# Performance work log

Hardware: AMD Instinct MI355X
Metric: run time of the kernel (lower is better)

The kernel has to match this reference:

```python
import jax, jax.numpy as jnp
import numpy as np

B, T, D, H = 2, 2048, 1024, 16
Dh = D // H


def _rope(q, k):
    # q, k: (B, H, T, Dh), interleaved even/odd rotation
    t = q.shape[2]
    dh = q.shape[3]
    inv_freq = 1.0 / (10000.0 ** (jnp.arange(0, dh, 2, dtype=jnp.float32) / dh))
    pos = jnp.arange(t, dtype=jnp.float32)
    freqs = pos[:, None] * inv_freq[None, :]          # (T, Dh/2)
    sin = jnp.sin(freqs)[None, None]                  # (1,1,T,Dh/2)
    cos = jnp.cos(freqs)[None, None]

    def rot(x):
        xe, xo = x[..., ::2], x[..., 1::2]
        re = xe * cos - xo * sin
        ro = xe * sin + xo * cos
        return jnp.stack([re, ro], axis=-1).reshape(x.shape)

    return rot(q), rot(k)


def setup_inputs() -> dict:
    key = jax.random.key(0)
    k1, k2, k3 = jax.random.split(key, 3)
    s = 1.0 / np.sqrt(D)
    return {
        "x": jax.random.normal(k1, (B, T, D), dtype=jnp.float32),
        "w_qkv": jax.random.normal(k2, (3 * D, D), dtype=jnp.float32) * s,
        "b_qkv": jnp.zeros((3 * D,), dtype=jnp.float32),
        "w_out": jax.random.normal(k3, (D, D), dtype=jnp.float32) * s,
        "b_out": jnp.zeros((D,), dtype=jnp.float32),
    }


def reference(x, w_qkv, b_qkv, w_out, b_out):
    b, t, d = x.shape
    qkv = x @ w_qkv.T + b_qkv                         # (B,T,3D)
    q, k, v = jnp.split(qkv, 3, axis=-1)
    q = q.reshape(b, t, H, Dh).transpose(0, 2, 1, 3)  # (B,H,T,Dh)
    k = k.reshape(b, t, H, Dh).transpose(0, 2, 1, 3)
    v = v.reshape(b, t, H, Dh).transpose(0, 2, 1, 3)
    q, k = _rope(q, k)
    scores = jnp.einsum("bhtd,bhsd->bhts", q, k) / jnp.sqrt(jnp.float32(Dh))
    causal = jnp.tril(jnp.ones((t, t), dtype=bool))[None, None]
    scores = jnp.where(causal, scores, -jnp.inf)
    probs = jax.nn.softmax(scores, axis=-1)
    out = jnp.einsum("bhts,bhsd->bhtd", probs, v)     # (B,H,T,Dh)
    out = out.transpose(0, 2, 1, 3).reshape(b, t, d)
    return out @ w_out.T + b_out
```

## Files before the change

kernel.cpp:

```cpp
#include <hip/hip_runtime.h>
#include <hip/hip_bf16.h>
#include <math.h>
#include <type_traits>

#define B_ 2
#define T_ 2048
#define D_ 1024
#define H_ 16
#define DH_ 64

typedef __bf16 bf16_t;
typedef bf16_t bf16x8 __attribute__((ext_vector_type(8)));
typedef bf16_t bf16x4 __attribute__((ext_vector_type(4)));
typedef float f32x4 __attribute__((ext_vector_type(4)));

typedef __attribute__((address_space(1))) const void gas_void;
typedef __attribute__((address_space(3))) void las_void;

__device__ __forceinline__ void gld16(const void* g, void* l) {
    __builtin_amdgcn_global_load_lds((gas_void*)g, (las_void*)l, 16, 0, 0);
}

#define WAITALL() asm volatile("s_waitcnt vmcnt(0) lgkmcnt(0)" ::: "memory")
#define BARRIER() do { asm volatile("" ::: "memory"); __builtin_amdgcn_s_barrier(); asm volatile("" ::: "memory"); } while (0)

__global__ __launch_bounds__(256) void cvt3(const float* __restrict__ a,
                                            const float* __restrict__ b,
                                            const float* __restrict__ c,
                                            bf16_t* __restrict__ oa,
                                            bf16_t* __restrict__ ob,
                                            bf16_t* __restrict__ oc,
                                            float2* __restrict__ tab) {
    if (blockIdx.x >= 8192) {
        int j = (blockIdx.x - 8192) * 256 + threadIdx.x;
        int t = j >> 5, d2 = j & 31;
        float invf = exp2f(-(float)d2 * 0.4152410118609203f);
        float ang = (float)t * invf;
        float sn, cs;
        sincosf(ang, &sn, &cs);
        tab[j] = make_float2(cs, sn);
        return;
    }
    int i = blockIdx.x * 256 + threadIdx.x;
    const float* src; bf16_t* dst; int off;
    if (i < 1048576)      { src = a; dst = oa; off = i; }
    else if (i < 1835008) { src = b; dst = ob; off = i - 1048576; }
    else                  { src = c; dst = oc; off = i - 1835008; }
    float4 f = ((const float4*)src)[off];
    bf16x4 v = { (bf16_t)f.x, (bf16_t)f.y, (bf16_t)f.z, (bf16_t)f.w };
    ((bf16x4*)dst)[off] = v;
}

__global__ __launch_bounds__(512, 4) void gemmqkv(const bf16_t* __restrict__ A,
                                                  const bf16_t* __restrict__ Bw,
                                                  const float* __restrict__ bias,
                                                  const float2* __restrict__ tab,
                                                  bf16_t* __restrict__ q_out,
                                                  bf16_t* __restrict__ k_out,
                                                  bf16_t* __restrict__ vt_out) {
    __shared__ __align__(16) char smem[65536];

    int tid = threadIdx.x;
    int lane = tid & 63, wid = tid >> 6;
    int wm = wid >> 2, wn = wid & 3;
    int lr = lane & 15, lk = lane >> 4;

    int l = blockIdx.y * 12 + blockIdx.x;
    int u = (l & 7) * 48 + (l >> 3);
    int bx = u % 12;
    int by = u / 12;

    f32x4 acc[4][4];
    f32x4 z = {0.f, 0.f, 0.f, 0.f};
#pragma unroll
    for (int i = 0; i < 4; i++)
#pragma unroll
        for (int j = 0; j < 4; j++) acc[i][j] = z;

    int cb = (tid & 3) * 16;
    int rT = tid >> 2;
    int sw = cb ^ (((rT >> 1) & 3) << 4);
    const char* gAp  = (const char*)A  + ((size_t)(by * 128 + rT)) * 2048 + sw;
    const char* gBp0 = (const char*)Bw + ((size_t)(bx * 256 + rT)) * 2048 + sw;
    const char* gBp1 = (const char*)Bw + ((size_t)(bx * 256 + 128 + rT)) * 2048 + sw;

    auto stg = [&](int par, int kt) __attribute__((always_inline)) {
        char* base = smem + par * 24576;
        gld16(gAp  + kt * 64, base + tid * 16);
        gld16(gBp0 + kt * 64, base + 8192 + tid * 16);
        gld16(gBp1 + kt * 64, base + 16384 + tid * 16);
    };

    int offA[4], offB[4];
#pragma unroll
    for (int m = 0; m < 4; m++) {
        int row = wm * 64 + m * 16 + lr;
        offA[m] = row * 64 + ((lk * 16) ^ (((row >> 1) & 3) << 4));
    }
#pragma unroll
    for (int n = 0; n < 4; n++) {
        int row = wn * 64 + n * 16 + lr;
        offB[n] = 8192 + row * 64 + ((lk * 16) ^ (((row >> 1) & 3) << 4));
    }

    stg(0, 0);
    for (int kt = 0; kt < 32; ++kt) {
        const char* buf = smem + (kt & 1) * 24576;
        WAITALL();
        BARRIER();
        if (kt < 31) stg((kt + 1) & 1, kt + 1);
        bf16x8 Af[4], Bf[4];
#pragma unroll
        for (int m = 0; m < 4; m++) Af[m] = *(const bf16x8*)(buf + offA[m]);
#pragma unroll
        for (int n = 0; n < 4; n++) Bf[n] = *(const bf16x8*)(buf + offB[n]);
        __builtin_amdgcn_s_setprio(1);
#pragma unroll
        for (int m = 0; m < 4; m++)
#pragma unroll
            for (int n = 0; n < 4; n++)
                acc[m][n] = __builtin_amdgcn_mfma_f32_16x16x32_bf16(Af[m], Bf[n], acc[m][n], 0, 0, 0);
        __builtin_amdgcn_s_setprio(0);
    }
    WAITALL();
    BARRIER();

    int m_base = by * 128 + wm * 64;
    int n_base = bx * 256 + wn * 64;
    char* myL = smem + wid * 8192;
    int which = n_base >> 10;
    int h = (n_base & 1023) >> 6;
    int b = m_base >> 11, t0 = m_base & 2047;
    int bh = b * H_ + h;
    if (which == 2) {
#pragma unroll
        for (int m = 0; m < 4; m++)
#pragma unroll
            for (int n = 0; n < 4; n++) {
                int rd = n * 16 + lr;
                float bv = bias[n_base + rd];
#pragma unroll
                for (int j = 0; j < 4; j++) {
                    int ct = m * 16 + lk * 4 + j;
                    int ct2 = (ct & 32) | (((ct >> 2) & 3) << 3) | (((ct >> 4) & 1) << 2) | (ct & 3);
                    int addr = (rd * 128 + ct2 * 2) ^ ((rd & 7) << 4);
                    *(bf16_t*)(myL + addr) = (bf16_t)(acc[m][n][j] + bv);
                }
            }
#pragma unroll
        for (int it = 0; it < 8; it++) {
            int row = it * 8 + (lane >> 3);
            int byt = (lane & 7) * 16;
            bf16x8 val = *(const bf16x8*)(myL + ((row * 128 + byt) ^ ((row & 7) << 4)));
            *(bf16x8*)(vt_out + ((size_t)bh * DH_ + row) * T_ + t0 + (lane & 7) * 8) = val;
        }
    } else {
        bf16_t* dst = which ? k_out : q_out;
        float qscl = which ? 1.0f : 0.18033688011112042f;
#pragma unroll
        for (int m = 0; m < 4; m++)
#pragma unroll
            for (int n = 0; n < 4; n++) {
                int dh = n * 16 + lr;
                float bv = bias[n_base + dh];
                int dh2 = dh >> 1;
                bool even = (dh & 1) == 0;
#pragma unroll
                for (int j = 0; j < 4; j++) {
                    int rt = m * 16 + lk * 4 + j;
                    float v = acc[m][n][j] + bv;
                    float pp = __shfl_xor(v, 1);
                    float2 cs = tab[(t0 + rt) * 32 + dh2];
                    float r = even ? v * cs.x - pp * cs.y : v * cs.x + pp * cs.y;
                    r *= qscl;
                    int addr = (rt * 128 + dh * 2) ^ ((rt & 7) << 4);
                    *(bf16_t*)(myL + addr) = (bf16_t)r;
                }
            }
#pragma unroll
        for (int it = 0; it < 8; it++) {
            int row = it * 8 + (lane >> 3);
            int byt = (lane & 7) * 16;
            bf16x8 val = *(const bf16x8*)(myL + ((row * 128 + byt) ^ ((row & 7) << 4)));
            *(bf16x8*)(dst + ((size_t)bh * T_ + t0 + row) * DH_ + (lane & 7) * 8) = val;
        }
    }
}

__global__ __launch_bounds__(256) void gemm128o(const bf16_t* __restrict__ A,
                                                const bf16_t* __restrict__ Bw,
                                                const float* __restrict__ bias,
                                                float* __restrict__ f_out,
                                                int K, int N) {
    __shared__ __align__(16) char smem[49152];
    char* b0 = smem;
    char* b1 = smem + 16384;
    char* b2 = smem + 32768;

    int tid = threadIdx.x;
    int lane = tid & 63, wid = tid >> 6;
    int wr = wid >> 1, wc = wid & 1;
    int lr = lane & 15, lk = lane >> 4;

    int l = blockIdx.y * gridDim.x + blockIdx.x;
    int chunk = (gridDim.x * gridDim.y) >> 3;
    int u = (l & 7) * chunk + (l >> 3);
    int bx = u % gridDim.x;
    int by = u / gridDim.x;

    f32x4 acc[4][4];
    f32x4 z = {0.f, 0.f, 0.f, 0.f};
#pragma unroll
    for (int i = 0; i < 4; i++)
#pragma unroll
        for (int j = 0; j < 4; j++) acc[i][j] = z;

    const char* Ab = (const char*)(A + (size_t)by * 128 * K);
    const char* Bb = (const char*)(Bw + (size_t)bx * 128 * K);
    const int rowstride = K * 2;

    int p0 = tid * 16;
    int p1 = 4096 + tid * 16;
    int r0 = p0 >> 6, r1 = p1 >> 6;
    int cb0 = (p0 & 63) ^ (((r0 >> 1) & 3) << 4);
    int cb1 = (p1 & 63) ^ (((r1 >> 1) & 3) << 4);
    size_t gA0 = (size_t)r0 * rowstride + cb0;
    size_t gA1 = (size_t)r1 * rowstride + cb1;

    int oa[4], ob[4];
#pragma unroll
    for (int m = 0; m < 4; m++) {
        int row = wr * 64 + m * 16 + lr;
        oa[m] = row * 64 + ((lk * 16) ^ (((row >> 1) & 3) << 4));
    }
#pragma unroll
    for (int n = 0; n < 4; n++) {
        int row = wc * 64 + n * 16 + lr;
        ob[n] = row * 64 + ((lk * 16) ^ (((row >> 1) & 3) << 4));
    }

    auto stg = [&](char* buf, int ks) __attribute__((always_inline)) {
        const char* Ag = Ab + (size_t)ks * 64;
        const char* Bg = Bb + (size_t)ks * 64;
        gld16(Ag + gA0, buf + p0);
        gld16(Ag + gA1, buf + p1);
        gld16(Bg + gA0, buf + 8192 + p0);
        gld16(Bg + gA1, buf + 8192 + p1);
    };

    auto iterf = [&](auto vmc, char* buf, int ks, bool dostage) __attribute__((always_inline)) {
        constexpr int VM = decltype(vmc)::value;
        if constexpr (VM == 8)      asm volatile("s_waitcnt vmcnt(8)" ::: "memory");
        else if constexpr (VM == 4) asm volatile("s_waitcnt vmcnt(4)" ::: "memory");
        else                        asm volatile("s_waitcnt vmcnt(0)" ::: "memory");
        __builtin_amdgcn_s_barrier();
        asm volatile("" ::: "memory");
        bf16x8 Af[4], Bf[4];
#pragma unroll
        for (int m = 0; m < 4; m++) Af[m] = *(const bf16x8*)(buf + oa[m]);
#pragma unroll
        for (int n = 0; n < 4; n++) Bf[n] = *(const bf16x8*)(buf + 8192 + ob[n]);
#pragma unroll
        for (int m = 0; m < 4; m++)
#pragma unroll
            for (int n = 0; n < 4; n++)
                acc[m][n] = __builtin_amdgcn_mfma_f32_16x16x32_bf16(Af[m], Bf[n], acc[m][n], 0, 0, 0);
        asm volatile("" ::: "memory");
        __builtin_amdgcn_s_barrier();
        asm volatile("" ::: "memory");
        if (dostage) stg(buf, ks);
    };

    std::integral_constant<int, 8> c8;
    std::integral_constant<int, 4> c4;
    std::integral_constant<int, 0> c0;

    stg(b0, 0);
    stg(b1, 1);
    stg(b2, 2);
    for (int s = 0; s < 30; s += 3) {
        iterf(c8, b0, s + 3, s + 3 < 32);
        iterf(c8, b1, s + 4, s + 4 < 32);
        iterf(c8, b2, s + 5, s + 5 < 32);
    }
    iterf(c4, b0, 0, false);
    iterf(c0, b1, 0, false);

    int m_base = by * 128 + wr * 64;
    int n_base = bx * 128 + wc * 64;
#pragma unroll
    for (int m = 0; m < 4; m++) {
        int gm0 = m_base + m * 16 + lk * 4;
#pragma unroll
        for (int n = 0; n < 4; n++) {
            int nc = n_base + n * 16 + lr;
            float bv = bias[nc];
#pragma unroll
            for (int j = 0; j < 4; j++)
                f_out[(size_t)(gm0 + j) * N + nc] = acc[m][n][j] + bv;
        }
    }
}

__global__ __launch_bounds__(256, 4) void attn128(const bf16_t* __restrict__ Q,
                                                  const bf16_t* __restrict__ K,
                                                  const bf16_t* __restrict__ Vt,
                                                  bf16_t* __restrict__ Ao) {
    __shared__ __align__(16) char smem[40960];

    int tid = threadIdx.x;
    int lane = tid & 63, wid = tid >> 6;
    int lr = lane & 15, lk = lane >> 4;
    int xcd = blockIdx.x & 7, idx = blockIdx.x >> 3;
    int bh = xcd * 4 + (idx & 3);
    int i4 = idx >> 2;
    int qt = (i4 < 8) ? i4 : 23 - i4;
    int q0 = qt * 128;
    int qrelw = wid * 16 + lr;

    const bf16_t* Qp0 = Q + ((size_t)bh * T_ + q0 + qrelw) * DH_;
    const bf16_t* Qp1 = Qp0 + 64 * DH_;
    bf16x8 qa0 = *(const bf16x8*)(Qp0 + lk * 8);
    bf16x8 qa1 = *(const bf16x8*)(Qp0 + 32 + lk * 8);
    bf16x8 qb0 = *(const bf16x8*)(Qp1 + lk * 8);
    bf16x8 qb1 = *(const bf16x8*)(Qp1 + 32 + lk * 8);

    f32x4 zz = {0.f, 0.f, 0.f, 0.f};
    f32x4 oa0[4], oa1[4];
#pragma unroll
    for (int dt = 0; dt < 4; dt++) { oa0[dt] = zz; oa1[dt] = zz; }
    float ls0 = 0.f, ls1 = 0.f;
    bf16x8 pA0, pA1, pB0, pB1;

    const char* Kbase = (const char*)(K + (size_t)bh * T_ * DH_);
    const char* Vbase = (const char*)(Vt + (size_t)bh * DH_ * T_);

    auto stage = [&](int s, char* Kd, char* Vd) __attribute__((always_inline)) {
        int kv0 = s * 64;
        const char* Kg = Kbase + (size_t)kv0 * 128;
#pragma unroll
        for (int c = 0; c < 2; c++) {
            int o = c * 4096 + tid * 16;
            int r = o >> 7;
            int g = o ^ ((r & 7) << 4);
            gld16(Kg + g, Kd + o);
            gld16(Vbase + (size_t)r * (T_ * 2) + kv0 * 2 + (g & 127), Vd + o);
        }
    };

    auto do_qk = [&](const char* Kc, int m0, int m1) __attribute__((always_inline)) {
#pragma unroll
        for (int kt = 0; kt < 4; kt++) {
            int row = kt * 16 + lr;
            int key = (row & 7) << 4;
            bf16x8 kf0 = *(const bf16x8*)(Kc + ((row * 128 + lk * 16) ^ key));
            bf16x8 kf1 = *(const bf16x8*)(Kc + ((row * 128 + 64 + lk * 16) ^ key));
            if (m0 != 2) {
                f32x4 s = zz;
                s = __builtin_amdgcn_mfma_f32_16x16x32_bf16(kf0, qa0, s, 0, 0, 0);
                s = __builtin_amdgcn_mfma_f32_16x16x32_bf16(kf1, qa1, s, 0, 0, 0);
#pragma unroll
                for (int j = 0; j < 4; j++) {
                    float sv = s[j];
                    if (m0 == 1) {
                        int kv = kt * 16 + lk * 4 + j;
                        sv = (kv <= qrelw) ? sv : -__builtin_inff();
                    }
                    float e = exp2f(sv);
                    ls0 += e;
                    if (kt < 2) pA0[kt * 4 + j] = (bf16_t)e;
                    else        pA1[(kt - 2) * 4 + j] = (bf16_t)e;
                }
            }
            {
                f32x4 s = zz;
                s = __builtin_amdgcn_mfma_f32_16x16x32_bf16(kf0, qb0, s, 0, 0, 0);
                s = __builtin_amdgcn_mfma_f32_16x16x32_bf16(kf1, qb1, s, 0, 0, 0);
#pragma unroll
                for (int j = 0; j < 4; j++) {
                    float sv = s[j];
                    if (m1 == 1) {
                        int kv = kt * 16 + lk * 4 + j;
                        sv = (kv <= qrelw) ? sv : -__builtin_inff();
                    }
                    float e = exp2f(sv);
                    ls1 += e;
                    if (kt < 2) pB0[kt * 4 + j] = (bf16_t)e;
                    else        pB1[(kt - 2) * 4 + j] = (bf16_t)e;
                }
            }
        }
    };

    auto do_pv = [&](const char* Vc, bool g0on) __attribute__((always_inline)) {
#pragma unroll
        for (int dt = 0; dt < 4; dt++) {
            int row = dt * 16 + lr;
            int key = (row & 7) << 4;
            bf16x8 vf0 = *(const bf16x8*)(Vc + ((row * 128 + lk * 16) ^ key));
            bf16x8 vf1 = *(const bf16x8*)(Vc + ((row * 128 + 64 + lk * 16) ^ key));
            if (g0on) {
                f32x4 o = oa0[dt];
                o = __builtin_amdgcn_mfma_f32_16x16x32_bf16(vf0, pA0, o, 0, 0, 0);
                o = __builtin_amdgcn_mfma_f32_16x16x32_bf16(vf1, pA1, o, 0, 0, 0);
                oa0[dt] = o;
            }
            f32x4 o = oa1[dt];
            o = __builtin_amdgcn_mfma_f32_16x16x32_bf16(vf0, pB0, o, 0, 0, 0);
            o = __builtin_amdgcn_mfma_f32_16x16x32_bf16(vf1, pB1, o, 0, 0, 0);
            oa1[dt] = o;
        }
    };

    stage(0, smem, smem + 16384);
    stage(1, smem + 8192, smem + 24576);
    asm volatile("s_waitcnt vmcnt(4)" ::: "memory");
    __builtin_amdgcn_s_barrier();
    asm volatile("" ::: "memory");
    do_qk(smem, qt == 0 ? 1 : 0, 0);

    char* Kr = smem + 8192;
    char* Kw = smem;
    char* Vr = smem + 16384;
    char* Vn = smem + 24576;
    char* Vw = smem + 32768;

    int last = 2 * qt;
    auto iterA = [&](int s, int m0, int m1) __attribute__((always_inline)) {
        WAITALL();
        __builtin_amdgcn_s_barrier();
        asm volatile("" ::: "memory");
        if (s + 2 <= last + 1) stage(s + 2, Kw, Vw);
        do_pv(Vr, true);
        do_qk(Kr, m0, m1);
        char* t;
        t = Kr; Kr = Kw; Kw = t;
        t = Vr; Vr = Vn; Vn = Vw; Vw = t;
    };

    for (int s = 0; s < last - 1; ++s) iterA(s, 0, 0);
    if (qt > 0) iterA(last - 1, 1, 0);
    iterA(last, 2, 1);
    do_pv(Vr, false);
    __syncthreads();

    ls0 += __shfl_xor(ls0, 16); ls0 += __shfl_xor(ls0, 32);
    ls1 += __shfl_xor(ls1, 16); ls1 += __shfl_xor(ls1, 32);
    float ri0 = __builtin_amdgcn_rcpf(ls0);
    float ri1 = __builtin_amdgcn_rcpf(ls1);

    char* myL = smem + wid * 2048;
    int b = bh >> 4, h = bh & 15;
#pragma unroll
    for (int dt = 0; dt < 4; dt++)
#pragma unroll
        for (int j = 0; j < 4; j++) {
            int dh = dt * 16 + lk * 4 + j;
            int addr = (lr * 128 + dh * 2) ^ ((lr & 7) << 4);
            *(bf16_t*)(myL + addr) = (bf16_t)(oa0[dt][j] * ri0);
        }
#pragma unroll
    for (int it = 0; it < 2; it++) {
        int row = it * 8 + (lane >> 3);
        int byt = (lane & 7) * 16;
        bf16x8 val = *(const bf16x8*)(myL + ((row * 128 + byt) ^ ((row & 7) << 4)));
        int t = q0 + wid * 16 + row;
        *(bf16x8*)(Ao + ((size_t)b * T_ + t) * D_ + h * DH_ + (lane & 7) * 8) = val;
    }
#pragma unroll
    for (int dt = 0; dt < 4; dt++)
#pragma unroll
        for (int j = 0; j < 4; j++) {
            int dh = dt * 16 + lk * 4 + j;
            int addr = (lr * 128 + dh * 2) ^ ((lr & 7) << 4);
            *(bf16_t*)(myL + addr) = (bf16_t)(oa1[dt][j] * ri1);
        }
#pragma unroll
    for (int it = 0; it < 2; it++) {
        int row = it * 8 + (lane >> 3);
        int byt = (lane & 7) * 16;
        bf16x8 val = *(const bf16x8*)(myL + ((row * 128 + byt) ^ ((row & 7) << 4)));
        int t = q0 + 64 + wid * 16 + row;
        *(bf16x8*)(Ao + ((size_t)b * T_ + t) * D_ + h * DH_ + (lane & 7) * 8) = val;
    }
}

extern "C" void kernel_launch(void* const* d_in, const int* in_sizes, int n_in,
                              void* d_out, int out_size, void* d_ws, size_t ws_size,
                              hipStream_t stream) {
    const float* x     = (const float*)d_in[0];
    const float* w_qkv = (const float*)d_in[1];
    const float* b_qkv = (const float*)d_in[2];
    const float* w_out = (const float*)d_in[3];
    const float* b_out = (const float*)d_in[4];
    float* out = (float*)d_out;

    char* ws = (char*)d_ws;
    bf16_t* xb    = (bf16_t*)(ws);
    bf16_t* wqkvb = (bf16_t*)(ws + 8388608);
    bf16_t* wob   = (bf16_t*)(ws + 14680064);
    bf16_t* qb    = (bf16_t*)(ws + 16777216);
    bf16_t* kb    = (bf16_t*)(ws + 25165824);
    bf16_t* vtb   = (bf16_t*)(ws + 33554432);
    bf16_t* ab    = (bf16_t*)(ws + 41943040);
    float2* tab   = (float2*)(ws + 41943040);

    cvt3<<<8448, 256, 0, stream>>>(x, w_qkv, w_out, xb, wqkvb, wob, tab);

    gemmqkv<<<dim3(12, 32), 512, 0, stream>>>(xb, wqkvb, b_qkv, tab, qb, kb, vtb);
    attn128<<<512, 256, 0, stream>>>(qb, kb, vtb, ab);
    gemm128o<<<dim3(8, 32), 256, 0, stream>>>(ab, wob, b_out, out, 1024, 1024);
}
```

Before: 108.7 us.

## Pair complementary query tiles per block with 128-wide KV chunks in attention

The attention kernel now gives each block two query tiles (qa and 15-qa) of the same head, so every block processes exactly 17 KV chunks and causal work is balanced. The grid shrinks to 256 blocks. KV chunks grow from 64 to 128 keys, with a triple-buffered V ring in a larger LDS allocation. Occupancy drops to one block of 256 threads per CU, which leaves fewer waves to hide latency, and on a large GPU 256 blocks may not fill every CU.

```diff
diff --git a/kernel.cpp b/kernel.cpp
--- a/kernel.cpp
+++ b/kernel.cpp
@@ -302,187 +302,187 @@
     }
 }
 
-__global__ __launch_bounds__(256, 4) void attn128(const bf16_t* __restrict__ Q,
+__global__ __launch_bounds__(256, 1) void attn256(const bf16_t* __restrict__ Q,
                                                   const bf16_t* __restrict__ K,
                                                   const bf16_t* __restrict__ Vt,
                                                   bf16_t* __restrict__ Ao) {
-    __shared__ __align__(16) char smem[40960];
+    __shared__ __align__(16) char smem[90112];
 
     int tid = threadIdx.x;
     int lane = tid & 63, wid = tid >> 6;
     int lr = lane & 15, lk = lane >> 4;
-    int xcd = blockIdx.x & 7, idx = blockIdx.x >> 3;
-    int bh = xcd * 4 + (idx & 3);
-    int i4 = idx >> 2;
-    int qt = (i4 < 8) ? i4 : 23 - i4;
-    int q0 = qt * 128;
+    int xcd = blockIdx.x & 7, i = blockIdx.x >> 3;
+    int bh = xcd * 4 + (i & 3);
+    int qa = i >> 2;
+    int qtA = qa, qtB = 15 - qa;
     int qrelw = wid * 16 + lr;
 
-    const bf16_t* Qp0 = Q + ((size_t)bh * T_ + q0 + qrelw) * DH_;
-    const bf16_t* Qp1 = Qp0 + 64 * DH_;
-    bf16x8 qa0 = *(const bf16x8*)(Qp0 + lk * 8);
-    bf16x8 qa1 = *(const bf16x8*)(Qp0 + 32 + lk * 8);
-    bf16x8 qb0 = *(const bf16x8*)(Qp1 + lk * 8);
-    bf16x8 qb1 = *(const bf16x8*)(Qp1 + 32 + lk * 8);
+    const bf16_t* QA = Q + ((size_t)bh * T_ + qtA * 128 + qrelw) * DH_;
+    const bf16_t* QB = Q + ((size_t)bh * T_ + qtB * 128 + qrelw) * DH_;
+    bf16x8 qAa0 = *(const bf16x8*)(QA + lk * 8);
+    bf16x8 qAa1 = *(const bf16x8*)(QA + 32 + lk * 8);
+    bf16x8 qAb0 = *(const bf16x8*)(QA + 64 * DH_ + lk * 8);
+    bf16x8 qAb1 = *(const bf16x8*)(QA + 64 * DH_ + 32 + lk * 8);
+    bf16x8 qBa0 = *(const bf16x8*)(QB + lk * 8);
+    bf16x8 qBa1 = *(const bf16x8*)(QB + 32 + lk * 8);
+    bf16x8 qBb0 = *(const bf16x8*)(QB + 64 * DH_ + lk * 8);
+    bf16x8 qBb1 = *(const bf16x8*)(QB + 64 * DH_ + 32 + lk * 8);
 
     f32x4 zz = {0.f, 0.f, 0.f, 0.f};
-    f32x4 oa0[4], oa1[4];
-#pragma unroll
-    for (int dt = 0; dt < 4; dt++) { oa0[dt] = zz; oa1[dt] = zz; }
+    f32x4 o0[4], o1[4];
+#pragma unroll
+    for (int dt = 0; dt < 4; dt++) { o0[dt] = zz; o1[dt] = zz; }
     float ls0 = 0.f, ls1 = 0.f;
-    bf16x8 pA0, pA1, pB0, pB1;
+    bf16x8 pA[4], pB[4];
 
     const char* Kbase = (const char*)(K + (size_t)bh * T_ * DH_);
     const char* Vbase = (const char*)(Vt + (size_t)bh * DH_ * T_);
 
-    auto stage = [&](int s, char* Kd, char* Vd) __attribute__((always_inline)) {
-        int kv0 = s * 64;
+    auto stage = [&](int slot) __attribute__((always_inline)) {
+        int ch = (slot <= qa) ? slot : slot - qa - 1;
+        int kv0 = ch * 128;
+        char* Kd = smem + (slot & 1) * 16384;
+        char* Vd = smem + 32768 + (slot % 3) * 16384;
         const char* Kg = Kbase + (size_t)kv0 * 128;
 #pragma unroll
-        for (int c = 0; c < 2; c++) {
-            int o = c * 4096 + tid * 16;
-            int r = o >> 7;
-            int g = o ^ ((r & 7) << 4);
-            gld16(Kg + g, Kd + o);
-            gld16(Vbase + (size_t)r * (T_ * 2) + kv0 * 2 + (g & 127), Vd + o);
-        }
-    };
-
-    auto do_qk = [&](const char* Kc, int m0, int m1) __attribute__((always_inline)) {
-#pragma unroll
-        for (int kt = 0; kt < 4; kt++) {
+        for (int ld = 0; ld < 4; ld++) {
+            int o = ld * 4096 + tid * 16;
+            int gk = o ^ (((o >> 7) & 7) << 4);
+            gld16(Kg + gk, Kd + o);
+            int rv = o >> 8, cv = o & 255;
+            int gv = cv ^ ((rv & 7) << 4);
+            gld16(Vbase + (size_t)rv * (T_ * 2) + kv0 * 2 + gv, Vd + o);
+        }
+    };
+
+    auto do_qk = [&](const char* Kc, bf16x8 qg0a, bf16x8 qg0b,
+                     bf16x8 qg1a, bf16x8 qg1b, bool dmask) __attribute__((always_inline)) {
+#pragma unroll
+        for (int kt = 0; kt < 8; kt++) {
             int row = kt * 16 + lr;
             int key = (row & 7) << 4;
             bf16x8 kf0 = *(const bf16x8*)(Kc + ((row * 128 + lk * 16) ^ key));
             bf16x8 kf1 = *(const bf16x8*)(Kc + ((row * 128 + 64 + lk * 16) ^ key));
-            if (m0 != 2) {
-                f32x4 s = zz;
-                s = __builtin_amdgcn_mfma_f32_16x16x32_bf16(kf0, qa0, s, 0, 0, 0);
-                s = __builtin_amdgcn_mfma_f32_16x16x32_bf16(kf1, qa1, s, 0, 0, 0);
-#pragma unroll
-                for (int j = 0; j < 4; j++) {
-                    float sv = s[j];
-                    if (m0 == 1) {
-                        int kv = kt * 16 + lk * 4 + j;
-                        sv = (kv <= qrelw) ? sv : -__builtin_inff();
-                    }
-                    float e = exp2f(sv);
-                    ls0 += e;
-                    if (kt < 2) pA0[kt * 4 + j] = (bf16_t)e;
-                    else        pA1[(kt - 2) * 4 + j] = (bf16_t)e;
+            f32x4 s = zz;
+            s = __builtin_amdgcn_mfma_f32_16x16x32_bf16(kf0, qg0a, s, 0, 0, 0);
+            s = __builtin_amdgcn_mfma_f32_16x16x32_bf16(kf1, qg0b, s, 0, 0, 0);
+#pragma unroll
+            for (int j = 0; j < 4; j++) {
+                float sv = s[j];
+                if (dmask) {
+                    int kvrel = kt * 16 + lk * 4 + j;
+                    sv = (kvrel <= qrelw) ? sv : -__builtin_inff();
                 }
+                float e = exp2f(sv);
+                ls0 += e;
+                pA[kt >> 1][(kt & 1) * 4 + j] = (bf16_t)e;
             }
-            {
-                f32x4 s = zz;
-                s = __builtin_amdgcn_mfma_f32_16x16x32_bf16(kf0, qb0, s, 0, 0, 0);
-                s = __builtin_amdgcn_mfma_f32_16x16x32_bf16(kf1, qb1, s, 0, 0, 0);
-#pragma unroll
-                for (int j = 0; j < 4; j++) {
-                    float sv = s[j];
-                    if (m1 == 1) {
-                        int kv = kt * 16 + lk * 4 + j;
-                        sv = (kv <= qrelw) ? sv : -__builtin_inff();
-                    }
-                    float e = exp2f(sv);
-                    ls1 += e;
-                    if (kt < 2) pB0[kt * 4 + j] = (bf16_t)e;
-                    else        pB1[(kt - 2) * 4 + j] = (bf16_t)e;
+            s = zz;
+            s = __builtin_amdgcn_mfma_f32_16x16x32_bf16(kf0, qg1a, s, 0, 0, 0);
+            s = __builtin_amdgcn_mfma_f32_16x16x32_bf16(kf1, qg1b, s, 0, 0, 0);
+#pragma unroll
+            for (int j = 0; j < 4; j++) {
+                float sv = s[j];
+                if (dmask) {
+                    int kvrel = kt * 16 + lk * 4 + j;
+                    sv = (kvrel <= 64 + qrelw) ? sv : -__builtin_inff();
                 }
+                float e = exp2f(sv);
+                ls1 += e;
+                pB[kt >> 1][(kt & 1) * 4 + j] = (bf16_t)e;
             }
         }
     };
 
-    auto do_pv = [&](const char* Vc, bool g0on) __attribute__((always_inline)) {
+    auto do_pv = [&](const char* Vc) __attribute__((always_inline)) {
 #pragma unroll
         for (int dt = 0; dt < 4; dt++) {
             int row = dt * 16 + lr;
             int key = (row & 7) << 4;
-            bf16x8 vf0 = *(const bf16x8*)(Vc + ((row * 128 + lk * 16) ^ key));
-            bf16x8 vf1 = *(const bf16x8*)(Vc + ((row * 128 + 64 + lk * 16) ^ key));
-            if (g0on) {
-                f32x4 o = oa0[dt];
-                o = __builtin_amdgcn_mfma_f32_16x16x32_bf16(vf0, pA0, o, 0, 0, 0);
-                o = __builtin_amdgcn_mfma_f32_16x16x32_bf16(vf1, pA1, o, 0, 0, 0);
-                oa0[dt] = o;
+            bf16x8 vf0 = *(const bf16x8*)(Vc + ((row * 256 + lk * 16) ^ key));
+            bf16x8 vf1 = *(const bf16x8*)(Vc + ((row * 256 + 64 + lk * 16) ^ key));
+            bf16x8 vf2 = *(const bf16x8*)(Vc + ((row * 256 + 128 + lk * 16) ^ key));
+            bf16x8 vf3 = *(const bf16x8*)(Vc + ((row * 256 + 192 + lk * 16) ^ key));
+            f32x4 a = o0[dt];
+            a = __builtin_amdgcn_mfma_f32_16x16x32_bf16(vf0, pA[0], a, 0, 0, 0);
+            a = __builtin_amdgcn_mfma_f32_16x16x32_bf16(vf1, pA[1], a, 0, 0, 0);
+            a = __builtin_amdgcn_mfma_f32_16x16x32_bf16(vf2, pA[2], a, 0, 0, 0);
+            a = __builtin_amdgcn_mfma_f32_16x16x32_bf16(vf3, pA[3], a, 0, 0, 0);
+            o0[dt] = a;
+            f32x4 b = o1[dt];
+            b = __builtin_amdgcn_mfma_f32_16x16x32_bf16(vf0, pB[0], b, 0, 0, 0);
+            b = __builtin_amdgcn_mfma_f32_16x16x32_bf16(vf1, pB[1], b, 0, 0, 0);
+            b = __builtin_amdgcn_mfma_f32_16x16x32_bf16(vf2, pB[2], b, 0, 0, 0);
+            b = __builtin_amdgcn_mfma_f32_16x16x32_bf16(vf3, pB[3], b, 0, 0, 0);
+            o1[dt] = b;
+        }
+    };
+
+    auto writeO = [&](int q0t) __attribute__((always_inline)) {
+        ls0 += __shfl_xor(ls0, 16); ls0 += __shfl_xor(ls0, 32);
+        ls1 += __shfl_xor(ls1, 16); ls1 += __shfl_xor(ls1, 32);
+        float ri0 = __builtin_amdgcn_rcpf(ls0);
+        float ri1 = __builtin_amdgcn_rcpf(ls1);
+        char* myL = smem + 81920 + wid * 2048;
+        int bb = bh >> 4, hh = bh & 15;
+#pragma unroll
+        for (int dt = 0; dt < 4; dt++)
+#pragma unroll
+            for (int j = 0; j < 4; j++) {
+                int dh = dt * 16 + lk * 4 + j;
+                int addr = (lr * 128 + dh * 2) ^ ((lr & 7) << 4);
+                *(bf16_t*)(myL + addr) = (bf16_t)(o0[dt][j] * ri0);
             }
-            f32x4 o = oa1[dt];
-            o = __builtin_amdgcn_mfma_f32_16x16x32_bf16(vf0, pB0, o, 0, 0, 0);
-            o = __builtin_amdgcn_mfma_f32_16x16x32_bf16(vf1, pB1, o, 0, 0, 0);
-            oa1[dt] = o;
-        }
-    };
-
-    stage(0, smem, smem + 16384);
-    stage(1, smem + 8192, smem + 24576);
-    asm volatile("s_waitcnt vmcnt(4)" ::: "memory");
-    __builtin_amdgcn_s_barrier();
-    asm volatile("" ::: "memory");
-    do_qk(smem, qt == 0 ? 1 : 0, 0);
-
-    char* Kr = smem + 8192;
-    char* Kw = smem;
-    char* Vr = smem + 16384;
-    char* Vn = smem + 24576;
-    char* Vw = smem + 32768;
-
-    int last = 2 * qt;
-    auto iterA = [&](int s, int m0, int m1) __attribute__((always_inline)) {
+#pragma unroll
+        for (int it = 0; it < 2; it++) {
+            int row = it * 8 + (lane >> 3);
+            int byt = (lane & 7) * 16;
+            bf16x8 val = *(const bf16x8*)(myL + ((row * 128 + byt) ^ ((row & 7) << 4)));
+            int t = q0t + wid * 16 + row;
+            *(bf16x8*)(Ao + ((size_t)bb * T_ + t) * D_ + hh * DH_ + (lane & 7) * 8) = val;
+        }
+#pragma unroll
+        for (int dt = 0; dt < 4; dt++)
+#pragma unroll
+            for (int j = 0; j < 4; j++) {
+                int dh = dt * 16 + lk * 4 + j;
+                int addr = (lr * 128 + dh * 2) ^ ((lr & 7) << 4);
+                *(bf16_t*)(myL + addr) = (bf16_t)(o1[dt][j] * ri1);
+            }
+#pragma unroll
+        for (int it = 0; it < 2; it++) {
+            int row = it * 8 + (lane >> 3);
+            int byt = (lane & 7) * 16;
+            bf16x8 val = *(const bf16x8*)(myL + ((row * 128 + byt) ^ ((row & 7) << 4)));
+            int t = q0t + 64 + wid * 16 + row;
+            *(bf16x8*)(Ao + ((size_t)bb * T_ + t) * D_ + hh * DH_ + (lane & 7) * 8) = val;
+        }
+    };
+
+    char* Vprev = smem + 32768 + 2 * 16384;
+    char* Vcur  = smem + 32768;
+    char* Vnext = smem + 32768 + 16384;
+
+    stage(0);
+    for (int slot = 0; slot <= 16; ++slot) {
         WAITALL();
-        __builtin_amdgcn_s_barrier();
-        asm volatile("" ::: "memory");
-        if (s + 2 <= last + 1) stage(s + 2, Kw, Vw);
-        do_pv(Vr, true);
-        do_qk(Kr, m0, m1);
-        char* t;
-        t = Kr; Kr = Kw; Kw = t;
-        t = Vr; Vr = Vn; Vn = Vw; Vw = t;
-    };
-
-    for (int s = 0; s < last - 1; ++s) iterA(s, 0, 0);
-    if (qt > 0) iterA(last - 1, 1, 0);
-    iterA(last, 2, 1);
-    do_pv(Vr, false);
-    __syncthreads();
-
-    ls0 += __shfl_xor(ls0, 16); ls0 += __shfl_xor(ls0, 32);
-    ls1 += __shfl_xor(ls1, 16); ls1 += __shfl_xor(ls1, 32);
-    float ri0 = __builtin_amdgcn_rcpf(ls0);
-    float ri1 = __builtin_amdgcn_rcpf(ls1);
-
-    char* myL = smem + wid * 2048;
-    int b = bh >> 4, h = bh & 15;
-#pragma unroll
-    for (int dt = 0; dt < 4; dt++)
-#pragma unroll
-        for (int j = 0; j < 4; j++) {
-            int dh = dt * 16 + lk * 4 + j;
-            int addr = (lr * 128 + dh * 2) ^ ((lr & 7) << 4);
-            *(bf16_t*)(myL + addr) = (bf16_t)(oa0[dt][j] * ri0);
-        }
-#pragma unroll
-    for (int it = 0; it < 2; it++) {
-        int row = it * 8 + (lane >> 3);
-        int byt = (lane & 7) * 16;
-        bf16x8 val = *(const bf16x8*)(myL + ((row * 128 + byt) ^ ((row & 7) << 4)));
-        int t = q0 + wid * 16 + row;
-        *(bf16x8*)(Ao + ((size_t)b * T_ + t) * D_ + h * DH_ + (lane & 7) * 8) = val;
-    }
-#pragma unroll
-    for (int dt = 0; dt < 4; dt++)
-#pragma unroll
-        for (int j = 0; j < 4; j++) {
-            int dh = dt * 16 + lk * 4 + j;
-            int addr = (lr * 128 + dh * 2) ^ ((lr & 7) << 4);
-            *(bf16_t*)(myL + addr) = (bf16_t)(oa1[dt][j] * ri1);
-        }
-#pragma unroll
-    for (int it = 0; it < 2; it++) {
-        int row = it * 8 + (lane >> 3);
-        int byt = (lane & 7) * 16;
-        bf16x8 val = *(const bf16x8*)(myL + ((row * 128 + byt) ^ ((row & 7) << 4)));
-        int t = q0 + 64 + wid * 16 + row;
-        *(bf16x8*)(Ao + ((size_t)b * T_ + t) * D_ + h * DH_ + (lane & 7) * 8) = val;
-    }
+        BARRIER();
+        if (slot < 16) stage(slot + 1);
+        if (slot > 0) do_pv(Vprev);
+        if (slot == qa + 1) {
+            writeO(qtA * 128);
+#pragma unroll
+            for (int dt = 0; dt < 4; dt++) { o0[dt] = zz; o1[dt] = zz; }
+            ls0 = 0.f; ls1 = 0.f;
+        }
+        const char* Kc = smem + (slot & 1) * 16384;
+        bool dm = (slot == qa) || (slot == 16);
+        if (slot <= qa) do_qk(Kc, qAa0, qAa1, qAb0, qAb1, dm);
+        else            do_qk(Kc, qBa0, qBa1, qBb0, qBb1, dm);
+        char* t = Vprev; Vprev = Vcur; Vcur = Vnext; Vnext = t;
+    }
+    do_pv(Vprev);
+    writeO(qtB * 128);
 }
 
 extern "C" void kernel_launch(void* const* d_in, const int* in_sizes, int n_in,
@@ -508,6 +508,6 @@
     cvt3<<<8448, 256, 0, stream>>>(x, w_qkv, w_out, xb, wqkvb, wob, tab);
 
     gemmqkv<<<dim3(12, 32), 512, 0, stream>>>(xb, wqkvb, b_qkv, tab, qb, kb, vtb);
-    attn128<<<512, 256, 0, stream>>>(qb, kb, vtb, ab);
+    attn256<<<256, 256, 0, stream>>>(qb, kb, vtb, ab);
     gemm128o<<<dim3(8, 32), 256, 0, stream>>>(ab, wob, b_out, out, 1024, 1024);
 }
```

After: 120.6 us. 1.11x slower.

## Split attention into 64-row query tiles with 2-wave blocks and tiered scheduling

Applied to the files above, without the earlier changes.

The attention kernel now uses 1024 blocks of 128 threads, each covering 64 query rows split into two 32-row groups per wave, instead of 512 blocks of 256 threads covering 128 rows. Block order is spread across four tiers so long and short causal tiles interleave for load balance. The KV loop is simplified to one 64-key stage per step with diagonal-only masking, and PV MFMAs run under raised wave priority. Smaller blocks should improve scheduling granularity and tail balance, but each block reloads the same K/V tiles, so more data is staged per query row, and the smem footprint stays at 40KB per block.

```diff
diff --git a/kernel.cpp b/kernel.cpp
--- a/kernel.cpp
+++ b/kernel.cpp
@@ -302,7 +302,7 @@
     }
 }
 
-__global__ __launch_bounds__(256, 4) void attn128(const bf16_t* __restrict__ Q,
+__global__ __launch_bounds__(128, 2) void attn64p(const bf16_t* __restrict__ Q,
                                                   const bf16_t* __restrict__ K,
                                                   const bf16_t* __restrict__ Vt,
                                                   bf16_t* __restrict__ Ao) {
@@ -311,19 +311,20 @@
     int tid = threadIdx.x;
     int lane = tid & 63, wid = tid >> 6;
     int lr = lane & 15, lk = lane >> 4;
-    int xcd = blockIdx.x & 7, idx = blockIdx.x >> 3;
-    int bh = xcd * 4 + (idx & 3);
-    int i4 = idx >> 2;
-    int qt = (i4 < 8) ? i4 : 23 - i4;
-    int q0 = qt * 128;
+    int bidx = blockIdx.x;
+    int xcd = bidx & 7;
+    int bh = xcd * 4 + ((bidx >> 3) & 3);
+    int qq = (bidx >> 5) & 7, tier = bidx >> 8;
+    int qt = (tier == 0) ? qq : (tier == 1) ? 31 - qq : (tier == 2) ? 8 + qq : 23 - qq;
+    int q0 = qt * 64;
     int qrelw = wid * 16 + lr;
 
-    const bf16_t* Qp0 = Q + ((size_t)bh * T_ + q0 + qrelw) * DH_;
-    const bf16_t* Qp1 = Qp0 + 64 * DH_;
-    bf16x8 qa0 = *(const bf16x8*)(Qp0 + lk * 8);
-    bf16x8 qa1 = *(const bf16x8*)(Qp0 + 32 + lk * 8);
-    bf16x8 qb0 = *(const bf16x8*)(Qp1 + lk * 8);
-    bf16x8 qb1 = *(const bf16x8*)(Qp1 + 32 + lk * 8);
+    const bf16_t* QA = Q + ((size_t)bh * T_ + q0 + qrelw) * DH_;
+    const bf16_t* QB = QA + 32 * DH_;
+    bf16x8 qa0 = *(const bf16x8*)(QA + lk * 8);
+    bf16x8 qa1 = *(const bf16x8*)(QA + 32 + lk * 8);
+    bf16x8 qb0 = *(const bf16x8*)(QB + lk * 8);
+    bf16x8 qb1 = *(const bf16x8*)(QB + 32 + lk * 8);
 
     f32x4 zz = {0.f, 0.f, 0.f, 0.f};
     f32x4 oa0[4], oa1[4];
@@ -339,8 +340,8 @@
         int kv0 = s * 64;
         const char* Kg = Kbase + (size_t)kv0 * 128;
 #pragma unroll
-        for (int c = 0; c < 2; c++) {
-            int o = c * 4096 + tid * 16;
+        for (int c = 0; c < 4; c++) {
+            int o = c * 2048 + tid * 16;
             int r = o >> 7;
             int g = o ^ ((r & 7) << 4);
             gld16(Kg + g, Kd + o);
@@ -348,101 +349,94 @@
         }
     };
 
-    auto do_qk = [&](const char* Kc, int m0, int m1) __attribute__((always_inline)) {
+    auto do_qk = [&](const char* Kc, bool dmask) __attribute__((always_inline)) {
 #pragma unroll
         for (int kt = 0; kt < 4; kt++) {
             int row = kt * 16 + lr;
             int key = (row & 7) << 4;
             bf16x8 kf0 = *(const bf16x8*)(Kc + ((row * 128 + lk * 16) ^ key));
             bf16x8 kf1 = *(const bf16x8*)(Kc + ((row * 128 + 64 + lk * 16) ^ key));
-            if (m0 != 2) {
-                f32x4 s = zz;
-                s = __builtin_amdgcn_mfma_f32_16x16x32_bf16(kf0, qa0, s, 0, 0, 0);
-                s = __builtin_amdgcn_mfma_f32_16x16x32_bf16(kf1, qa1, s, 0, 0, 0);
-#pragma unroll
-                for (int j = 0; j < 4; j++) {
-                    float sv = s[j];
-                    if (m0 == 1) {
-                        int kv = kt * 16 + lk * 4 + j;
-                        sv = (kv <= qrelw) ? sv : -__builtin_inff();
-                    }
-                    float e = exp2f(sv);
-                    ls0 += e;
-                    if (kt < 2) pA0[kt * 4 + j] = (bf16_t)e;
-                    else        pA1[(kt - 2) * 4 + j] = (bf16_t)e;
+            f32x4 s = zz;
+            s = __builtin_amdgcn_mfma_f32_16x16x32_bf16(kf0, qa0, s, 0, 0, 0);
+            s = __builtin_amdgcn_mfma_f32_16x16x32_bf16(kf1, qa1, s, 0, 0, 0);
+#pragma unroll
+            for (int j = 0; j < 4; j++) {
+                float sv = s[j];
+                if (dmask) {
+                    int kv = kt * 16 + lk * 4 + j;
+                    sv = (kv <= qrelw) ? sv : -__builtin_inff();
                 }
+                float e = exp2f(sv);
+                ls0 += e;
+                if (kt < 2) pA0[kt * 4 + j] = (bf16_t)e;
+                else        pA1[(kt - 2) * 4 + j] = (bf16_t)e;
             }
-            {
-                f32x4 s = zz;
-                s = __builtin_amdgcn_mfma_f32_16x16x32_bf16(kf0, qb0, s, 0, 0, 0);
-                s = __builtin_amdgcn_mfma_f32_16x16x32_bf16(kf1, qb1, s, 0, 0, 0);
-#pragma unroll
-                for (int j = 0; j < 4; j++) {
-                    float sv = s[j];
-                    if (m1 == 1) {
-                        int kv = kt * 16 + lk * 4 + j;
-                        sv = (kv <= qrelw) ? sv : -__builtin_inff();
-                    }
-                    float e = exp2f(sv);
-                    ls1 += e;
-                    if (kt < 2) pB0[kt * 4 + j] = (bf16_t)e;
-                    else        pB1[(kt - 2) * 4 + j] = (bf16_t)e;
+            s = zz;
+            s = __builtin_amdgcn_mfma_f32_16x16x32_bf16(kf0, qb0, s, 0, 0, 0);
+            s = __builtin_amdgcn_mfma_f32_16x16x32_bf16(kf1, qb1, s, 0, 0, 0);
+#pragma unroll
+            for (int j = 0; j < 4; j++) {
+                float sv = s[j];
+                if (dmask) {
+                    int kv = kt * 16 + lk * 4 + j;
+                    sv = (kv <= 32 + qrelw) ? sv : -__builtin_inff();
                 }
+                float e = exp2f(sv);
+                ls1 += e;
+                if (kt < 2) pB0[kt * 4 + j] = (bf16_t)e;
+                else        pB1[(kt - 2) * 4 + j] = (bf16_t)e;
             }
         }
     };
 
-    auto do_pv = [&](const char* Vc, bool g0on) __attribute__((always_inline)) {
+    auto do_pv = [&](const char* Vc) __attribute__((always_inline)) {
+        __builtin_amdgcn_s_setprio(1);
 #pragma unroll
         for (int dt = 0; dt < 4; dt++) {
             int row = dt * 16 + lr;
             int key = (row & 7) << 4;
             bf16x8 vf0 = *(const bf16x8*)(Vc + ((row * 128 + lk * 16) ^ key));
             bf16x8 vf1 = *(const bf16x8*)(Vc + ((row * 128 + 64 + lk * 16) ^ key));
-            if (g0on) {
-                f32x4 o = oa0[dt];
-                o = __builtin_amdgcn_mfma_f32_16x16x32_bf16(vf0, pA0, o, 0, 0, 0);
-                o = __builtin_amdgcn_mfma_f32_16x16x32_bf16(vf1, pA1, o, 0, 0, 0);
-                oa0[dt] = o;
-            }
-            f32x4 o = oa1[dt];
-            o = __builtin_amdgcn_mfma_f32_16x16x32_bf16(vf0, pB0, o, 0, 0, 0);
-            o = __builtin_amdgcn_mfma_f32_16x16x32_bf16(vf1, pB1, o, 0, 0, 0);
-            oa1[dt] = o;
-        }
+            f32x4 a = oa0[dt];
+            a = __builtin_amdgcn_mfma_f32_16x16x32_bf16(vf0, pA0, a, 0, 0, 0);
+            a = __builtin_amdgcn_mfma_f32_16x16x32_bf16(vf1, pA1, a, 0, 0, 0);
+            oa0[dt] = a;
+            f32x4 b = oa1[dt];
+            b = __builtin_amdgcn_mfma_f32_16x16x32_bf16(vf0, pB0, b, 0, 0, 0);
+            b = __builtin_amdgcn_mfma_f32_16x16x32_bf16(vf1, pB1, b, 0, 0, 0);
+            oa1[dt] = b;
+        }
+        __builtin_amdgcn_s_setprio(0);
     };
 
-    stage(0, smem, smem + 16384);
-    stage(1, smem + 8192, smem + 24576);
-    asm volatile("s_waitcnt vmcnt(4)" ::: "memory");
-    __builtin_amdgcn_s_barrier();
-    asm volatile("" ::: "memory");
-    do_qk(smem, qt == 0 ? 1 : 0, 0);
-
-    char* Kr = smem + 8192;
-    char* Kw = smem;
-    char* Vr = smem + 16384;
-    char* Vn = smem + 24576;
-    char* Vw = smem + 32768;
-
-    int last = 2 * qt;
-    auto iterA = [&](int s, int m0, int m1) __attribute__((always_inline)) {
+    char* Kcur = smem + 8192;
+    char* Kalt = smem;
+    char* Vprev = smem + 16384;
+    char* Vcur  = smem + 24576;
+    char* Vnext = smem + 32768;
+
+    stage(0, Kalt, Vprev);
+    if (qt > 0) {
+        stage(1, Kcur, Vcur);
+        asm volatile("s_waitcnt vmcnt(8)" ::: "memory");
+    } else {
         WAITALL();
-        __builtin_amdgcn_s_barrier();
-        asm volatile("" ::: "memory");
-        if (s + 2 <= last + 1) stage(s + 2, Kw, Vw);
-        do_pv(Vr, true);
-        do_qk(Kr, m0, m1);
-        char* t;
-        t = Kr; Kr = Kw; Kw = t;
-        t = Vr; Vr = Vn; Vn = Vw; Vw = t;
-    };
-
-    for (int s = 0; s < last - 1; ++s) iterA(s, 0, 0);
-    if (qt > 0) iterA(last - 1, 1, 0);
-    iterA(last, 2, 1);
-    do_pv(Vr, false);
-    __syncthreads();
+    }
+    BARRIER();
+    do_qk(Kalt, qt == 0);
+
+    for (int s = 1; s <= qt; ++s) {
+        WAITALL();
+        BARRIER();
+        if (s < qt) stage(s + 1, Kalt, Vnext);
+        do_pv(Vprev);
+        do_qk(Kcur, s == qt);
+        char* t = Kcur; Kcur = Kalt; Kalt = t;
+        t = Vprev; Vprev = Vcur; Vcur = Vnext; Vnext = t;
+    }
+    do_pv(Vprev);
+    WAITALL();
+    BARRIER();
 
     ls0 += __shfl_xor(ls0, 16); ls0 += __shfl_xor(ls0, 32);
     ls1 += __shfl_xor(ls1, 16); ls1 += __shfl_xor(ls1, 32);
@@ -450,7 +444,7 @@
     float ri1 = __builtin_amdgcn_rcpf(ls1);
 
     char* myL = smem + wid * 2048;
-    int b = bh >> 4, h = bh & 15;
+    int bb = bh >> 4, hh = bh & 15;
 #pragma unroll
     for (int dt = 0; dt < 4; dt++)
 #pragma unroll
@@ -465,7 +459,7 @@
         int byt = (lane & 7) * 16;
         bf16x8 val = *(const bf16x8*)(myL + ((row * 128 + byt) ^ ((row & 7) << 4)));
         int t = q0 + wid * 16 + row;
-        *(bf16x8*)(Ao + ((size_t)b * T_ + t) * D_ + h * DH_ + (lane & 7) * 8) = val;
+        *(bf16x8*)(Ao + ((size_t)bb * T_ + t) * D_ + hh * DH_ + (lane & 7) * 8) = val;
     }
 #pragma unroll
     for (int dt = 0; dt < 4; dt++)
@@ -480,8 +474,8 @@
         int row = it * 8 + (lane >> 3);
         int byt = (lane & 7) * 16;
         bf16x8 val = *(const bf16x8*)(myL + ((row * 128 + byt) ^ ((row & 7) << 4)));
-        int t = q0 + 64 + wid * 16 + row;
-        *(bf16x8*)(Ao + ((size_t)b * T_ + t) * D_ + h * DH_ + (lane & 7) * 8) = val;
+        int t = q0 + 32 + wid * 16 + row;
+        *(bf16x8*)(Ao + ((size_t)bb * T_ + t) * D_ + hh * DH_ + (lane & 7) * 8) = val;
     }
 }
 
@@ -508,6 +502,6 @@
     cvt3<<<8448, 256, 0, stream>>>(x, w_qkv, w_out, xb, wqkvb, wob, tab);
 
     gemmqkv<<<dim3(12, 32), 512, 0, stream>>>(xb, wqkvb, b_qkv, tab, qb, kb, vtb);
-    attn128<<<512, 256, 0, stream>>>(qb, kb, vtb, ab);
+    attn64p<<<1024, 128, 0, stream>>>(qb, kb, vtb, ab);
     gemm128o<<<dim3(8, 32), 256, 0, stream>>>(ab, wob, b_out, out, 1024, 1024);
 }
```

After: 116.2 us. 1.07x slower.

## Interleave QK softmax and PV MFMAs with double-buffered P registers

Applied to the files above, without the earlier changes.

Merges the QK^T/exp step for the next KV tile and the PV accumulation for the previous tile into one loop over 16-row subtiles. Two sets of P registers are used in ping-pong fashion, and the loop is unrolled by two so the compiler can hold them in registers. The goal is to let MFMA work overlap the exp/convert VALU work and the LDS reads, instead of running PV and QK as separate phases. The cost is more VGPRs from the second P buffer, which may lower occupancy, and more complex last-iteration masking logic.

```diff
diff --git a/kernel.cpp b/kernel.cpp
--- a/kernel.cpp
+++ b/kernel.cpp
@@ -330,10 +330,17 @@
 #pragma unroll
     for (int dt = 0; dt < 4; dt++) { oa0[dt] = zz; oa1[dt] = zz; }
     float ls0 = 0.f, ls1 = 0.f;
-    bf16x8 pA0, pA1, pB0, pB1;
+    bf16x8 PA0_0, PA1_0, PB0_0, PB1_0;
+    bf16x8 PA0_1, PA1_1, PB0_1, PB1_1;
 
     const char* Kbase = (const char*)(K + (size_t)bh * T_ * DH_);
     const char* Vbase = (const char*)(Vt + (size_t)bh * DH_ * T_);
+
+    char* Kr = smem + 8192;
+    char* Kw = smem;
+    char* Vr = smem + 16384;
+    char* Vn = smem + 24576;
+    char* Vw = smem + 32768;
 
     auto stage = [&](int s, char* Kd, char* Vd) __attribute__((always_inline)) {
         int kv0 = s * 64;
@@ -348,14 +355,16 @@
         }
     };
 
-    auto do_qk = [&](const char* Kc, int m0, int m1) __attribute__((always_inline)) {
+    auto do_qk = [&](const char* Kc, int m0, int m1,
+                     bf16x8& wA0, bf16x8& wA1, bf16x8& wB0, bf16x8& wB1)
+                 __attribute__((always_inline)) {
 #pragma unroll
         for (int kt = 0; kt < 4; kt++) {
             int row = kt * 16 + lr;
             int key = (row & 7) << 4;
             bf16x8 kf0 = *(const bf16x8*)(Kc + ((row * 128 + lk * 16) ^ key));
             bf16x8 kf1 = *(const bf16x8*)(Kc + ((row * 128 + 64 + lk * 16) ^ key));
-            if (m0 != 2) {
+            {
                 f32x4 s = zz;
                 s = __builtin_amdgcn_mfma_f32_16x16x32_bf16(kf0, qa0, s, 0, 0, 0);
                 s = __builtin_amdgcn_mfma_f32_16x16x32_bf16(kf1, qa1, s, 0, 0, 0);
@@ -368,8 +377,8 @@
                     }
                     float e = exp2f(sv);
                     ls0 += e;
-                    if (kt < 2) pA0[kt * 4 + j] = (bf16_t)e;
-                    else        pA1[(kt - 2) * 4 + j] = (bf16_t)e;
+                    if (kt < 2) wA0[kt * 4 + j] = (bf16_t)e;
+                    else        wA1[(kt - 2) * 4 + j] = (bf16_t)e;
                 }
             }
             {
@@ -385,63 +394,106 @@
                     }
                     float e = exp2f(sv);
                     ls1 += e;
-                    if (kt < 2) pB0[kt * 4 + j] = (bf16_t)e;
-                    else        pB1[(kt - 2) * 4 + j] = (bf16_t)e;
+                    if (kt < 2) wB0[kt * 4 + j] = (bf16_t)e;
+                    else        wB1[(kt - 2) * 4 + j] = (bf16_t)e;
                 }
             }
         }
     };
 
-    auto do_pv = [&](const char* Vc, bool g0on) __attribute__((always_inline)) {
-#pragma unroll
-        for (int dt = 0; dt < 4; dt++) {
-            int row = dt * 16 + lr;
-            int key = (row & 7) << 4;
-            bf16x8 vf0 = *(const bf16x8*)(Vc + ((row * 128 + lk * 16) ^ key));
-            bf16x8 vf1 = *(const bf16x8*)(Vc + ((row * 128 + 64 + lk * 16) ^ key));
-            if (g0on) {
-                f32x4 o = oa0[dt];
-                o = __builtin_amdgcn_mfma_f32_16x16x32_bf16(vf0, pA0, o, 0, 0, 0);
-                o = __builtin_amdgcn_mfma_f32_16x16x32_bf16(vf1, pA1, o, 0, 0, 0);
-                oa0[dt] = o;
-            }
-            f32x4 o = oa1[dt];
-            o = __builtin_amdgcn_mfma_f32_16x16x32_bf16(vf0, pB0, o, 0, 0, 0);
-            o = __builtin_amdgcn_mfma_f32_16x16x32_bf16(vf1, pB1, o, 0, 0, 0);
-            oa1[dt] = o;
-        }
-    };
-
-    stage(0, smem, smem + 16384);
-    stage(1, smem + 8192, smem + 24576);
-    asm volatile("s_waitcnt vmcnt(4)" ::: "memory");
-    __builtin_amdgcn_s_barrier();
-    asm volatile("" ::: "memory");
-    do_qk(smem, qt == 0 ? 1 : 0, 0);
-
-    char* Kr = smem + 8192;
-    char* Kw = smem;
-    char* Vr = smem + 16384;
-    char* Vn = smem + 24576;
-    char* Vw = smem + 32768;
-
     int last = 2 * qt;
-    auto iterA = [&](int s, int m0, int m1) __attribute__((always_inline)) {
+
+    auto iterX = [&](int s, int m0, int m1,
+                     bf16x8& rA0, bf16x8& rA1, bf16x8& rB0, bf16x8& rB1,
+                     bf16x8& wA0, bf16x8& wA1, bf16x8& wB0, bf16x8& wB1)
+                 __attribute__((always_inline)) {
         WAITALL();
         __builtin_amdgcn_s_barrier();
         asm volatile("" ::: "memory");
         if (s + 2 <= last + 1) stage(s + 2, Kw, Vw);
-        do_pv(Vr, true);
-        do_qk(Kr, m0, m1);
-        char* t;
-        t = Kr; Kr = Kw; Kw = t;
+#pragma unroll
+        for (int i = 0; i < 4; i++) {
+            int row = i * 16 + lr;
+            int key = (row & 7) << 4;
+            bf16x8 kf0 = *(const bf16x8*)(Kr + ((row * 128 + lk * 16) ^ key));
+            bf16x8 kf1 = *(const bf16x8*)(Kr + ((row * 128 + 64 + lk * 16) ^ key));
+            if (m0 != 2) {
+                f32x4 s_ = zz;
+                s_ = __builtin_amdgcn_mfma_f32_16x16x32_bf16(kf0, qa0, s_, 0, 0, 0);
+                s_ = __builtin_amdgcn_mfma_f32_16x16x32_bf16(kf1, qa1, s_, 0, 0, 0);
+#pragma unroll
+                for (int j = 0; j < 4; j++) {
+                    float sv = s_[j];
+                    if (m0 == 1) {
+                        int kv = i * 16 + lk * 4 + j;
+                        sv = (kv <= qrelw) ? sv : -__builtin_inff();
+                    }
+                    float e = exp2f(sv);
+                    ls0 += e;
+                    if (i < 2) wA0[i * 4 + j] = (bf16_t)e;
+                    else       wA1[(i - 2) * 4 + j] = (bf16_t)e;
+                }
+            }
+            {
+                f32x4 s_ = zz;
+                s_ = __builtin_amdgcn_mfma_f32_16x16x32_bf16(kf0, qb0, s_, 0, 0, 0);
+                s_ = __builtin_amdgcn_mfma_f32_16x16x32_bf16(kf1, qb1, s_, 0, 0, 0);
+#pragma unroll
+                for (int j = 0; j < 4; j++) {
+                    float sv = s_[j];
+                    if (m1 == 1) {
+                        int kv = i * 16 + lk * 4 + j;
+                        sv = (kv <= qrelw) ? sv : -__builtin_inff();
+                    }
+                    float e = exp2f(sv);
+                    ls1 += e;
+                    if (i < 2) wB0[i * 4 + j] = (bf16_t)e;
+                    else       wB1[(i - 2) * 4 + j] = (bf16_t)e;
+                }
+            }
+            bf16x8 vf0 = *(const bf16x8*)(Vr + ((row * 128 + lk * 16) ^ key));
+            bf16x8 vf1 = *(const bf16x8*)(Vr + ((row * 128 + 64 + lk * 16) ^ key));
+            f32x4 a = oa0[i];
+            a = __builtin_amdgcn_mfma_f32_16x16x32_bf16(vf0, rA0, a, 0, 0, 0);
+            a = __builtin_amdgcn_mfma_f32_16x16x32_bf16(vf1, rA1, a, 0, 0, 0);
+            oa0[i] = a;
+            f32x4 b = oa1[i];
+            b = __builtin_amdgcn_mfma_f32_16x16x32_bf16(vf0, rB0, b, 0, 0, 0);
+            b = __builtin_amdgcn_mfma_f32_16x16x32_bf16(vf1, rB1, b, 0, 0, 0);
+            oa1[i] = b;
+        }
+        char* t = Kr; Kr = Kw; Kw = t;
         t = Vr; Vr = Vn; Vn = Vw; Vw = t;
     };
 
-    for (int s = 0; s < last - 1; ++s) iterA(s, 0, 0);
-    if (qt > 0) iterA(last - 1, 1, 0);
-    iterA(last, 2, 1);
-    do_pv(Vr, false);
+    stage(0, Kw, Vr);
+    stage(1, Kr, Vn);
+    asm volatile("s_waitcnt vmcnt(4)" ::: "memory");
+    __builtin_amdgcn_s_barrier();
+    asm volatile("" ::: "memory");
+    do_qk(Kw, qt == 0 ? 1 : 0, 0, PA0_0, PA1_0, PB0_0, PB1_0);
+
+    for (int s = 0; s < last; s += 2) {
+        iterX(s,     0, 0,
+              PA0_0, PA1_0, PB0_0, PB1_0, PA0_1, PA1_1, PB0_1, PB1_1);
+        iterX(s + 1, (s + 1 == last - 1) ? 1 : 0, 0,
+              PA0_1, PA1_1, PB0_1, PB1_1, PA0_0, PA1_0, PB0_0, PB1_0);
+    }
+    iterX(last, 2, 1,
+          PA0_0, PA1_0, PB0_0, PB1_0, PA0_1, PA1_1, PB0_1, PB1_1);
+    {
+#pragma unroll
+        for (int dt = 0; dt < 4; dt++) {
+            int row = dt * 16 + lr;
+            int key = (row & 7) << 4;
+            bf16x8 vf0 = *(const bf16x8*)(Vr + ((row * 128 + lk * 16) ^ key));
+            bf16x8 vf1 = *(const bf16x8*)(Vr + ((row * 128 + 64 + lk * 16) ^ key));
+            f32x4 o = oa1[dt];
+            o = __builtin_amdgcn_mfma_f32_16x16x32_bf16(vf0, PB0_1, o, 0, 0, 0);
+            o = __builtin_amdgcn_mfma_f32_16x16x32_bf16(vf1, PB1_1, o, 0, 0, 0);
+            oa1[dt] = o;
+        }
+    }
     __syncthreads();
 
     ls0 += __shfl_xor(ls0, 16); ls0 += __shfl_xor(ls0, 32);
```

Measured after the change: 105.6 us. 2.8% less time.
